# Optimization experiments

Hardware: AMD Instinct MI355X
Metric: run time of the kernel (lower is better)

The kernel has to match this reference:

```python
import jax, jax.numpy as jnp
import numpy as np

NEG_BIG = -9e15  # matches torch's -9000000000000000.0 masked-fill value
ALPHA = 0.2      # LeakyReLU negative slope


def setup_inputs() -> dict:
    key = jax.random.key(0)
    k1, k2, k3, k4 = jax.random.split(key, 4)
    N, F_in, F_out = 8192, 128, 64
    h = jax.random.normal(k1, (N, F_in), dtype=jnp.float32)
    adj = jax.random.randint(k2, (N, N), 0, 2).astype(jnp.float32)
    # Glorot(gain=1.414)-scale params
    W = jax.random.normal(k3, (F_in, F_out), dtype=jnp.float32) * (1.414 * np.sqrt(2.0 / (F_in + F_out)))
    a = jax.random.normal(k4, (2 * F_out, 1), dtype=jnp.float32) * (1.414 * np.sqrt(2.0 / (2 * F_out + 1)))
    return {"h": h, "adj": adj, "W": W, "a": a}


def reference(h, adj, W, a):
    F_out = W.shape[1]
    Wh = h @ W                               # [N, F_out]
    Wh1 = Wh @ a[:F_out, :]                  # [N, 1]
    Wh2 = Wh @ a[F_out:, :]                  # [N, 1]
    e = jax.nn.leaky_relu(Wh1 + Wh2.T, negative_slope=ALPHA)  # [N, N]
    attention = jnp.where(adj > 0, e, NEG_BIG)
    attention = jax.nn.softmax(attention, axis=1)
    # dropout omitted (eval mode / p applied only in training)
    h_prime = attention @ Wh                 # [N, F_out]
    return jax.nn.elu(h_prime)               # concat=True -> ELU
```

## Files before the change

### kernel.cpp

```cpp
#include <hip/hip_runtime.h>
#include <hip/hip_bf16.h>

#define N 8192
#define FIN 128
#define FOUT 64
#define ALPHA 0.2f
#define LOG2E 1.44269504f
#define STJ 256
#define NSTAGES (N / STJ)
#define RS 260

typedef __attribute__((ext_vector_type(8))) short short8;
typedef __attribute__((ext_vector_type(4))) float f32x4;

static __device__ __forceinline__ unsigned fkey(float x) {
    unsigned u = __float_as_uint(x);
    return (u >> 31) ? ~u : (u | 0x80000000u);
}
static __device__ __forceinline__ float fdecode(unsigned k) {
    unsigned u = (k & 0x80000000u) ? (k & 0x7FFFFFFFu) : ~k;
    return __uint_as_float(u);
}

static __device__ __forceinline__ void gll16(const float* g, float* l) {
    __builtin_amdgcn_global_load_lds(
        (const __attribute__((address_space(1))) unsigned int*)g,
        (__attribute__((address_space(3))) unsigned int*)l, 16, 0, 0);
}

__global__ __launch_bounds__(256) void k_prep(const float* __restrict__ h,
                                              const float* __restrict__ W,
                                              const float* __restrict__ a,
                                              float* __restrict__ Wh,
                                              float* __restrict__ s,
                                              float* __restrict__ t,
                                              unsigned* __restrict__ keys) {
    __shared__ float lH[16 * FIN];
    __shared__ float lW[FIN * FOUT];
    __shared__ float red[8];
    const int tid = threadIdx.x;
    const int r0 = blockIdx.x * 16;
    {
        const float4* src = (const float4*)(h + (size_t)r0 * FIN);
        float4* dst = (float4*)lH;
        for (int i = tid; i < 16 * FIN / 4; i += 256) dst[i] = src[i];
        const float4* ws_ = (const float4*)W;
        float4* dw = (float4*)lW;
        for (int i = tid; i < FIN * FOUT / 4; i += 256) dw[i] = ws_[i];
    }
    __syncthreads();
    const int wave = tid >> 6, lane = tid & 63;
    float acc[4] = {0.f, 0.f, 0.f, 0.f};
    for (int k = 0; k < FIN; ++k) {
        float wv = lW[k * FOUT + lane];
#pragma unroll
        for (int r = 0; r < 4; ++r)
            acc[r] = fmaf(lH[(wave * 4 + r) * FIN + k], wv, acc[r]);
    }
    const float a1 = a[lane], a2 = a[FOUT + lane];
    float smx = -1e30f, tmx = -1e30f;
#pragma unroll
    for (int r = 0; r < 4; ++r) {
        int row = r0 + wave * 4 + r;
        Wh[(size_t)row * FOUT + lane] = acc[r];
        float sv = acc[r] * a1, tv = acc[r] * a2;
#pragma unroll
        for (int off = 32; off; off >>= 1) {
            sv += __shfl_xor(sv, off);
            tv += __shfl_xor(tv, off);
        }
        if (lane == 0) { s[row] = sv; t[row] = tv; }
        smx = fmaxf(smx, sv);
        tmx = fmaxf(tmx, tv);
    }
    if (lane == 0) { red[wave] = smx; red[4 + wave] = tmx; }
    __syncthreads();
    if (tid == 0) {
        float ms = fmaxf(fmaxf(red[0], red[1]), fmaxf(red[2], red[3]));
        float mt = fmaxf(fmaxf(red[4], red[5]), fmaxf(red[6], red[7]));
        atomicMax(keys + 0, fkey(ms));
        atomicMax(keys + 1, fkey(mt));
    }
}

__global__ __launch_bounds__(256) void k_pack(const float* __restrict__ Wh,
                                              __hip_bfloat16* __restrict__ WhB) {
    const int c = blockIdx.x;
    const int tn = threadIdx.x >> 6;
    const int lane = threadIdx.x & 63;
    const int quad = lane >> 4, l16 = lane & 15;
    const float* src = Wh + ((size_t)(c * 32 + quad * 8)) * FOUT + tn * 16 + l16;
    union { unsigned short u[8]; short8 v; } frag;
#pragma unroll
    for (int e = 0; e < 8; ++e) {
        __hip_bfloat16 b = __float2bfloat16(src[(size_t)e * FOUT]);
        frag.u[e] = *(unsigned short*)&b;
    }
    *(short8*)&WhB[(((size_t)c * 4 + tn) * 64 + lane) * 8] = frag.v;
}

__global__ __launch_bounds__(512) void k_attn(const float* __restrict__ adj,
                                              const __hip_bfloat16* __restrict__ WhB,
                                              const float* __restrict__ s,
                                              const float* __restrict__ t,
                                              const unsigned* __restrict__ keys,
                                              float* __restrict__ out) {
    __shared__ float bufA[2][16 * RS];
    __shared__ float bufT[2][STJ];
    __shared__ float shacc[8][64][4];
    __shared__ float shl[2][16];
    const int wave = threadIdx.x >> 6, lane = threadIdx.x & 63;
    const int quad = lane >> 4, l16 = lane & 15;
    const int ct = wave & 3, jh = wave >> 2;
    const int i0 = blockIdx.x * 16;

    const float mraw = fdecode(keys[0]) + fdecode(keys[1]);
    const float mle = mraw > 0.f ? mraw : ALPHA * mraw;
    const float mm = mle * LOG2E;
    const float sm = s[i0 + l16];
    const short8* BF = (const short8*)WhB;

    f32x4 acc = {0, 0, 0, 0};
    float lsum = 0.f;

    const int r2 = 2 * wave;
    const float* gadj = adj + (size_t)(i0 + r2) * N + lane * 4;

    gll16(gadj, &bufA[0][r2 * RS]);
    gll16(gadj + N, &bufA[0][(r2 + 1) * RS]);
    if (wave == 0) gll16(t + lane * 4, &bufT[0][0]);
    __syncthreads();

    for (int st = 0; st < NSTAGES; ++st) {
        const int b = st & 1;
        if (st + 1 < NSTAGES) {
            const float* g = gadj + (size_t)(st + 1) * STJ;
            gll16(g, &bufA[b ^ 1][r2 * RS]);
            gll16(g + N, &bufA[b ^ 1][(r2 + 1) * RS]);
            if (wave == 0) gll16(t + (size_t)(st + 1) * STJ + lane * 4, &bufT[b ^ 1][0]);
        }
        const float* A = &bufA[b][0];
        const float* T = &bufT[b][0];
        const int cbase = st * 8 + jh * 4;
        short8 Bf0 = BF[((cbase + 0) * 4 + ct) * 64 + lane];
        short8 Bf1 = BF[((cbase + 1) * 4 + ct) * 64 + lane];
        short8 Bf2 = BF[((cbase + 2) * 4 + ct) * 64 + lane];
        short8 Bf3 = BF[((cbase + 3) * 4 + ct) * 64 + lane];
#pragma unroll
        for (int u = 0; u < 4; ++u) {
            const int j0 = jh * 128 + u * 32 + quad * 8;
            float4 a0 = *(const float4*)&A[l16 * RS + j0];
            float4 a1 = *(const float4*)&A[l16 * RS + j0 + 4];
            float4 t0 = *(const float4*)&T[j0];
            float4 t1 = *(const float4*)&T[j0 + 4];
            union { unsigned short u16[8]; short8 v; } af;
#pragma unroll
            for (int e = 0; e < 8; ++e) {
                float av = (e < 4) ? ((const float*)&a0)[e] : ((const float*)&a1)[e - 4];
                float tv = (e < 4) ? ((const float*)&t0)[e] : ((const float*)&t1)[e - 4];
                float x = sm + tv;
                float le = fmaxf(x, ALPHA * x);
                float ex = exp2f(fmaf(le, LOG2E, -mm));
                float p = av * ex;
                __hip_bfloat16 pb = __float2bfloat16(p);
                unsigned short ub = *(unsigned short*)&pb;
                af.u16[e] = ub;
                lsum += __uint_as_float(((unsigned)ub) << 16);
            }
            const short8 bb = (u == 0) ? Bf0 : (u == 1) ? Bf1 : (u == 2) ? Bf2 : Bf3;
            acc = __builtin_amdgcn_mfma_f32_16x16x32_bf16(af.v, bb, acc, 0, 0, 0);
        }
        __syncthreads();
    }

    lsum += __shfl_xor(lsum, 16);
    lsum += __shfl_xor(lsum, 32);
#pragma unroll
    for (int r = 0; r < 4; ++r) shacc[wave][lane][r] = acc[r];
    if (ct == 0 && lane < 16) shl[jh][lane] = lsum;
    __syncthreads();

    if (wave < 4) {
#pragma unroll
        for (int r = 0; r < 4; ++r) {
            float tot = shacc[wave][lane][r] + shacc[wave + 4][lane][r];
            int row = quad * 4 + r;
            float l = shl[0][row] + shl[1][row];
            float v = tot / l;
            float o = v > 0.f ? v : (exp2f(v * LOG2E) - 1.f);
            out[(size_t)(i0 + row) * FOUT + wave * 16 + l16] = o;
        }
    }
}

extern "C" void kernel_launch(void* const* d_in, const int* in_sizes, int n_in,
                              void* d_out, int out_size, void* d_ws, size_t ws_size,
                              hipStream_t stream) {
    const float* h   = (const float*)d_in[0];
    const float* adj = (const float*)d_in[1];
    const float* W   = (const float*)d_in[2];
    const float* a   = (const float*)d_in[3];
    float* out = (float*)d_out;

    float* Wh = (float*)d_ws;
    __hip_bfloat16* WhB = (__hip_bfloat16*)(Wh + (size_t)N * FOUT);
    float* s = (float*)(WhB + (size_t)N * FOUT);
    float* t = s + N;
    unsigned* keys = (unsigned*)(t + N);

    hipMemsetAsync(keys, 0, 2 * sizeof(unsigned), stream);
    k_prep<<<N / 16, 256, 0, stream>>>(h, W, a, Wh, s, t, keys);
    k_pack<<<N / 32, 256, 0, stream>>>(Wh, WhB);
    k_attn<<<N / 16, 512, 0, stream>>>(adj, WhB, s, t, keys, out);
}
```

Measured before the change: 429.6 us.

## Split attention over column chunks with atomic accumulation and final normalize kernel

The attention kernel now splits the N columns into four chunks across a second grid dimension. Each block has four waves, and each wave covers 32 columns per stage while computing all four output tiles with four MFMAs sharing one A fragment. Partial numerators and row sums are combined with global atomicAdd into a zeroed workspace, and a new k_final kernel applies the normalization and ELU. LOG2E is also folded into s and t in the prep kernel, which saves a multiply per element. The change raises the number of blocks and parallelism for the memory-bound adj stream, at the cost of atomics, an extra memset and an extra launch.

```diff
diff --git a/kernel.cpp b/kernel.cpp
--- a/kernel.cpp
+++ b/kernel.cpp
@@ -6,9 +6,10 @@
 #define FOUT 64
 #define ALPHA 0.2f
 #define LOG2E 1.44269504f
-#define STJ 256
-#define NSTAGES (N / STJ)
-#define RS 260
+#define JSPLIT 4
+#define JSPAN (N / JSPLIT)
+#define STJ 128
+#define NST (JSPAN / STJ)
 
 typedef __attribute__((ext_vector_type(8))) short short8;
 typedef __attribute__((ext_vector_type(4))) float f32x4;
@@ -21,7 +22,6 @@
     unsigned u = (k & 0x80000000u) ? (k & 0x7FFFFFFFu) : ~k;
     return __uint_as_float(u);
 }
-
 static __device__ __forceinline__ void gll16(const float* g, float* l) {
     __builtin_amdgcn_global_load_lds(
         (const __attribute__((address_space(1))) unsigned int*)g,
@@ -32,8 +32,8 @@
                                               const float* __restrict__ W,
                                               const float* __restrict__ a,
                                               float* __restrict__ Wh,
-                                              float* __restrict__ s,
-                                              float* __restrict__ t,
+                                              float* __restrict__ s2,
+                                              float* __restrict__ t2,
                                               unsigned* __restrict__ keys) {
     __shared__ float lH[16 * FIN];
     __shared__ float lW[FIN * FOUT];
@@ -69,7 +69,8 @@
             sv += __shfl_xor(sv, off);
             tv += __shfl_xor(tv, off);
         }
-        if (lane == 0) { s[row] = sv; t[row] = tv; }
+        sv *= LOG2E; tv *= LOG2E;
+        if (lane == 0) { s2[row] = sv; t2[row] = tv; }
         smx = fmaxf(smx, sv);
         tmx = fmaxf(tmx, tv);
     }
@@ -99,98 +100,122 @@
     *(short8*)&WhB[(((size_t)c * 4 + tn) * 64 + lane) * 8] = frag.v;
 }
 
-__global__ __launch_bounds__(512) void k_attn(const float* __restrict__ adj,
+__global__ __launch_bounds__(256) void k_attn(const float* __restrict__ adj,
                                               const __hip_bfloat16* __restrict__ WhB,
-                                              const float* __restrict__ s,
-                                              const float* __restrict__ t,
+                                              const float* __restrict__ s2,
+                                              const float* __restrict__ t2,
                                               const unsigned* __restrict__ keys,
-                                              float* __restrict__ out) {
-    __shared__ float bufA[2][16 * RS];
-    __shared__ float bufT[2][STJ];
-    __shared__ float shacc[8][64][4];
-    __shared__ float shl[2][16];
+                                              float* __restrict__ acc_ws,
+                                              float* __restrict__ l_ws) {
+    __shared__ float smem[2 * 4 * 512];
+    __shared__ float smT[2][256];
+    __shared__ float shl[4][16];
     const int wave = threadIdx.x >> 6, lane = threadIdx.x & 63;
     const int quad = lane >> 4, l16 = lane & 15;
-    const int ct = wave & 3, jh = wave >> 2;
     const int i0 = blockIdx.x * 16;
+    const int jbase = blockIdx.y * JSPAN;
 
     const float mraw = fdecode(keys[0]) + fdecode(keys[1]);
-    const float mle = mraw > 0.f ? mraw : ALPHA * mraw;
-    const float mm = mle * LOG2E;
-    const float sm = s[i0 + l16];
+    const float mm = mraw > 0.f ? mraw : ALPHA * mraw;
+    const float sm = s2[i0 + l16];
     const short8* BF = (const short8*)WhB;
 
-    f32x4 acc = {0, 0, 0, 0};
+    const float* ga = adj + (size_t)(i0 + l16) * N + jbase + wave * 32 + quad * 8;
+    const float* gt = t2 + jbase + lane * 4;
+
+    f32x4 acc0 = {0,0,0,0}, acc1 = {0,0,0,0}, acc2 = {0,0,0,0}, acc3 = {0,0,0,0};
     float lsum = 0.f;
 
-    const int r2 = 2 * wave;
-    const float* gadj = adj + (size_t)(i0 + r2) * N + lane * 4;
-
-    gll16(gadj, &bufA[0][r2 * RS]);
-    gll16(gadj + N, &bufA[0][(r2 + 1) * RS]);
-    if (wave == 0) gll16(t + lane * 4, &bufT[0][0]);
-    __syncthreads();
-
-    for (int st = 0; st < NSTAGES; ++st) {
+    gll16(ga, smem + wave * 512);
+    gll16(ga + 4, smem + wave * 512 + 256);
+    if (wave == 0) gll16(gt, smT[0]);
+    __syncthreads();
+
+    for (int st = 0; st < NST; ++st) {
         const int b = st & 1;
-        if (st + 1 < NSTAGES) {
-            const float* g = gadj + (size_t)(st + 1) * STJ;
-            gll16(g, &bufA[b ^ 1][r2 * RS]);
-            gll16(g + N, &bufA[b ^ 1][(r2 + 1) * RS]);
-            if (wave == 0) gll16(t + (size_t)(st + 1) * STJ + lane * 4, &bufT[b ^ 1][0]);
+        if (st + 1 < NST) {
+            const float* g = ga + (size_t)(st + 1) * STJ;
+            float* lb = smem + (b ^ 1) * 2048 + wave * 512;
+            gll16(g, lb);
+            gll16(g + 4, lb + 256);
+            if (wave == 0) gll16(gt + (size_t)(st + 1) * STJ, smT[b ^ 1]);
         }
-        const float* A = &bufA[b][0];
-        const float* T = &bufT[b][0];
-        const int cbase = st * 8 + jh * 4;
-        short8 Bf0 = BF[((cbase + 0) * 4 + ct) * 64 + lane];
-        short8 Bf1 = BF[((cbase + 1) * 4 + ct) * 64 + lane];
-        short8 Bf2 = BF[((cbase + 2) * 4 + ct) * 64 + lane];
-        short8 Bf3 = BF[((cbase + 3) * 4 + ct) * 64 + lane];
-#pragma unroll
-        for (int u = 0; u < 4; ++u) {
-            const int j0 = jh * 128 + u * 32 + quad * 8;
-            float4 a0 = *(const float4*)&A[l16 * RS + j0];
-            float4 a1 = *(const float4*)&A[l16 * RS + j0 + 4];
-            float4 t0 = *(const float4*)&T[j0];
-            float4 t1 = *(const float4*)&T[j0 + 4];
-            union { unsigned short u16[8]; short8 v; } af;
-#pragma unroll
-            for (int e = 0; e < 8; ++e) {
-                float av = (e < 4) ? ((const float*)&a0)[e] : ((const float*)&a1)[e - 4];
-                float tv = (e < 4) ? ((const float*)&t0)[e] : ((const float*)&t1)[e - 4];
-                float x = sm + tv;
-                float le = fmaxf(x, ALPHA * x);
-                float ex = exp2f(fmaf(le, LOG2E, -mm));
-                float p = av * ex;
-                __hip_bfloat16 pb = __float2bfloat16(p);
-                unsigned short ub = *(unsigned short*)&pb;
-                af.u16[e] = ub;
-                lsum += __uint_as_float(((unsigned)ub) << 16);
-            }
-            const short8 bb = (u == 0) ? Bf0 : (u == 1) ? Bf1 : (u == 2) ? Bf2 : Bf3;
-            acc = __builtin_amdgcn_mfma_f32_16x16x32_bf16(af.v, bb, acc, 0, 0, 0);
+        const int kc = blockIdx.y * (JSPAN / 32) + st * 4 + wave;
+        short8 Bf0 = BF[((size_t)kc * 4 + 0) * 64 + lane];
+        short8 Bf1 = BF[((size_t)kc * 4 + 1) * 64 + lane];
+        short8 Bf2 = BF[((size_t)kc * 4 + 2) * 64 + lane];
+        short8 Bf3 = BF[((size_t)kc * 4 + 3) * 64 + lane];
+        const float* Au = smem + b * 2048 + wave * 512;
+        float4 alo = *(const float4*)(Au + (lane << 2));
+        float4 ahi = *(const float4*)(Au + 256 + (lane << 2));
+        const float* Tu = smT[b] + wave * 32 + quad * 8;
+        float4 tlo = *(const float4*)(Tu);
+        float4 thi = *(const float4*)(Tu + 4);
+
+        union { __hip_bfloat162 h2[4]; short8 v; } af;
+#pragma unroll
+        for (int pp = 0; pp < 4; ++pp) {
+            float a0 = (pp < 2) ? ((const float*)&alo)[2 * pp]     : ((const float*)&ahi)[2 * pp - 4];
+            float a1 = (pp < 2) ? ((const float*)&alo)[2 * pp + 1] : ((const float*)&ahi)[2 * pp - 3];
+            float t0 = (pp < 2) ? ((const float*)&tlo)[2 * pp]     : ((const float*)&thi)[2 * pp - 4];
+            float t1 = (pp < 2) ? ((const float*)&tlo)[2 * pp + 1] : ((const float*)&thi)[2 * pp - 3];
+            float x0 = sm + t0,            x1 = sm + t1;
+            float le0 = fmaxf(x0, ALPHA * x0), le1 = fmaxf(x1, ALPHA * x1);
+            float p0 = a0 * exp2f(le0 - mm),   p1 = a1 * exp2f(le1 - mm);
+            __hip_bfloat162 pb = __float22bfloat162_rn(make_float2(p0, p1));
+            af.h2[pp] = pb;
+            lsum += __bfloat162float(pb.x) + __bfloat162float(pb.y);
         }
+        acc0 = __builtin_amdgcn_mfma_f32_16x16x32_bf16(af.v, Bf0, acc0, 0, 0, 0);
+        acc1 = __builtin_amdgcn_mfma_f32_16x16x32_bf16(af.v, Bf1, acc1, 0, 0, 0);
+        acc2 = __builtin_amdgcn_mfma_f32_16x16x32_bf16(af.v, Bf2, acc2, 0, 0, 0);
+        acc3 = __builtin_amdgcn_mfma_f32_16x16x32_bf16(af.v, Bf3, acc3, 0, 0, 0);
         __syncthreads();
     }
 
     lsum += __shfl_xor(lsum, 16);
     lsum += __shfl_xor(lsum, 32);
-#pragma unroll
-    for (int r = 0; r < 4; ++r) shacc[wave][lane][r] = acc[r];
-    if (ct == 0 && lane < 16) shl[jh][lane] = lsum;
-    __syncthreads();
-
-    if (wave < 4) {
-#pragma unroll
-        for (int r = 0; r < 4; ++r) {
-            float tot = shacc[wave][lane][r] + shacc[wave + 4][lane][r];
-            int row = quad * 4 + r;
-            float l = shl[0][row] + shl[1][row];
-            float v = tot / l;
-            float o = v > 0.f ? v : (exp2f(v * LOG2E) - 1.f);
-            out[(size_t)(i0 + row) * FOUT + wave * 16 + l16] = o;
-        }
-    }
+
+    float* accr = smem;
+    *(f32x4*)&accr[((wave * 4 + 0) * 64 + lane) * 4] = acc0;
+    *(f32x4*)&accr[((wave * 4 + 1) * 64 + lane) * 4] = acc1;
+    *(f32x4*)&accr[((wave * 4 + 2) * 64 + lane) * 4] = acc2;
+    *(f32x4*)&accr[((wave * 4 + 3) * 64 + lane) * 4] = acc3;
+    if (lane < 16) shl[wave][lane] = lsum;
+    __syncthreads();
+
+    const int tile = wave;
+    f32x4 tot = {0, 0, 0, 0};
+#pragma unroll
+    for (int w = 0; w < 4; ++w) {
+        f32x4 c = *(const f32x4*)&accr[((w * 4 + tile) * 64 + lane) * 4];
+        tot[0] += c[0]; tot[1] += c[1]; tot[2] += c[2]; tot[3] += c[3];
+    }
+#pragma unroll
+    for (int r = 0; r < 4; ++r) {
+        int row = quad * 4 + r;
+        atomicAdd(&acc_ws[(size_t)(i0 + row) * FOUT + tile * 16 + l16], tot[r]);
+    }
+    if (wave == 0 && lane < 16) {
+        float lv = shl[0][lane] + shl[1][lane] + shl[2][lane] + shl[3][lane];
+        atomicAdd(&l_ws[i0 + lane], lv);
+    }
+}
+
+__global__ __launch_bounds__(256) void k_final(const float* __restrict__ acc_ws,
+                                               const float* __restrict__ l_ws,
+                                               float* __restrict__ out) {
+    const int idx = blockIdx.x * 256 + threadIdx.x;
+    const int row = idx >> 4;
+    const float inv = 1.0f / l_ws[row];
+    float4 a = ((const float4*)acc_ws)[idx];
+    float4 o;
+#pragma unroll
+    for (int r = 0; r < 4; ++r) {
+        float v = ((const float*)&a)[r] * inv;
+        ((float*)&o)[r] = v > 0.f ? v : (exp2f(v * LOG2E) - 1.f);
+    }
+    ((float4*)out)[idx] = o;
 }
 
 extern "C" void kernel_launch(void* const* d_in, const int* in_sizes, int n_in,
@@ -204,12 +229,18 @@
 
     float* Wh = (float*)d_ws;
     __hip_bfloat16* WhB = (__hip_bfloat16*)(Wh + (size_t)N * FOUT);
-    float* s = (float*)(WhB + (size_t)N * FOUT);
-    float* t = s + N;
-    unsigned* keys = (unsigned*)(t + N);
-
-    hipMemsetAsync(keys, 0, 2 * sizeof(unsigned), stream);
-    k_prep<<<N / 16, 256, 0, stream>>>(h, W, a, Wh, s, t, keys);
+    float* s2 = (float*)(WhB + (size_t)N * FOUT);
+    float* t2 = s2 + N;
+    float* pad = t2 + N;
+    float* acc_ws = pad + 256;
+    float* l_ws = acc_ws + (size_t)N * FOUT;
+    unsigned* keys = (unsigned*)(l_ws + N);
+
+    hipMemsetAsync(acc_ws, 0, ((size_t)N * FOUT + N) * sizeof(float) + 2 * sizeof(unsigned),
+                   stream);
+    k_prep<<<N / 16, 256, 0, stream>>>(h, W, a, Wh, s2, t2, keys);
     k_pack<<<N / 32, 256, 0, stream>>>(Wh, WhB);
-    k_attn<<<N / 16, 512, 0, stream>>>(adj, WhB, s, t, keys, out);
-}
+    dim3 ag(N / 16, JSPLIT);
+    k_attn<<<ag, 256, 0, stream>>>(adj, WhB, s2, t2, keys, acc_ws, l_ws);
+    k_final<<<(N * FOUT / 4) / 256, 256, 0, stream>>>(acc_ws, l_ws, out);
+}
```

New measurement: 415.7 us. 1.03x faster.
